# Performance work log

Measured on AMD Instinct MI355X. Metric: run time of the kernel, lower is better.

The kernel has to match this reference:

```python
import jax, jax.numpy as jnp
import numpy as np

N0, N1, N2 = 200000, 50000, 10000
E1, E2 = 800000, 160000
IN_F, HID, RANK, OUT_C = 128, 128, 64, 64


def _cp_graphconv(feat_src, feat_dst, src, dst, n_dst, W_src, W_dst, W_out, b):
    # CP-rank factorized GraphConv: project src feats to rank space, gather along
    # edges, mean-aggregate per dst node, multiply elementwise with dst rank
    # projection (CP / Hadamard fusion), then project to output space.
    h_src = feat_src @ W_src                      # [N_src, R]
    msg = h_src[src]                              # [E, R] gather
    agg = jax.ops.segment_sum(msg, dst, num_segments=n_dst)   # [n_dst, R]
    cnt = jax.ops.segment_sum(jnp.ones((dst.shape[0],), msg.dtype), dst, num_segments=n_dst)
    agg = agg / jnp.maximum(cnt, 1.0)[:, None]    # mean aggregation
    z = agg * (feat_dst @ W_dst)                  # [n_dst, R] CP hadamard
    return z @ W_out + b                          # [n_dst, out]


def setup_inputs() -> dict:
    key = jax.random.key(0)
    ks = jax.random.split(key, 12)
    s1 = 1.0 / np.sqrt(IN_F)
    s2 = 1.0 / np.sqrt(HID)
    sr = 1.0 / np.sqrt(RANK)
    return {
        "x": jax.random.normal(ks[0], (N0, IN_F), jnp.float32),
        "W_src1": jax.random.normal(ks[1], (IN_F, RANK), jnp.float32) * s1,
        "W_dst1": jax.random.normal(ks[2], (IN_F, RANK), jnp.float32) * s1,
        "W_out1": jax.random.normal(ks[3], (RANK, HID), jnp.float32) * sr,
        "b1": jnp.zeros((HID,), jnp.float32),
        "W_src2": jax.random.normal(ks[4], (HID, RANK), jnp.float32) * s2,
        "W_dst2": jax.random.normal(ks[5], (HID, RANK), jnp.float32) * s2,
        "W_out2": jax.random.normal(ks[6], (RANK, OUT_C), jnp.float32) * sr,
        "b2": jnp.zeros((OUT_C,), jnp.float32),
        "src1": jax.random.randint(ks[7], (E1,), 0, N0),
        "dst1": jax.random.randint(ks[8], (E1,), 0, N1),
        "src2": jax.random.randint(ks[9], (E2,), 0, N1),
        "dst2": jax.random.randint(ks[10], (E2,), 0, N2),
        "n_dst1": N1,
        "n_dst2": N2,
    }


def reference(x, W_src1, W_dst1, W_out1, b1, W_src2, W_dst2, W_out2, b2,
              src1, dst1, src2, dst2, n_dst1, n_dst2):
    h_dst = x[:n_dst1]
    h = _cp_graphconv(x, h_dst, src1, dst1, n_dst1, W_src1, W_dst1, W_out1, b1)
    h = jax.nn.relu(h)
    # dropout: eval mode (training=False) -> identity
    h_dst2 = h[:n_dst2]
    out = _cp_graphconv(h, h_dst2, src2, dst2, n_dst2, W_src2, W_dst2, W_out2, b2)
    return out
```

## Files before the change

### kernel.cpp

```cpp
#include <hip/hip_runtime.h>
#include <hip/hip_bf16.h>
#include <hip/hip_fp16.h>

#define N0 200000
#define N1 50000
#define N2 10000
#define E1C 800000
#define E2C 160000
#define NB1 784
#define NB2 160
#define NBT (NB1 + NB2)
#define CH1 64
#define CH2 16
#define NT1 3125
#define NT2 625

struct H4 { __half2 a, b; };
struct H8 { __half2 a, b, c, d; };

typedef _Float16 f16x8 __attribute__((ext_vector_type(8)));
typedef float f32x4 __attribute__((ext_vector_type(4)));
#define MFMA16(a, b, c) __builtin_amdgcn_mfma_f32_16x16x32_f16(a, b, c, 0, 0, 0)

#define WT_TOTAL 45056

__global__ __launch_bounds__(256) void prep(int4* __restrict__ histz,
                                            const float4* __restrict__ x4,
                                            H4* __restrict__ xh4,
                                            const float* __restrict__ Wsrc1,
                                            const float* __restrict__ Wdst1,
                                            const float* __restrict__ Wout1,
                                            const float* __restrict__ Wsrc2,
                                            const float* __restrict__ Wdst2,
                                            const float* __restrict__ Wout2,
                                            __half* __restrict__ wt) {
    const int NZ4 = NBT / 4;
    const int NC = N0 * 128 / 4;
    int i = blockIdx.x * 256 + threadIdx.x;
    if (i < NZ4) {
        histz[i] = make_int4(0, 0, 0, 0);
    } else {
        int j = i - NZ4;
        if (j < NC) {
            float4 v = x4[j];
            H4 o;
            o.a = __floats2half2_rn(v.x, v.y);
            o.b = __floats2half2_rn(v.z, v.w);
            xh4[j] = o;
        } else {
            int e = j - NC;
            if (e < WT_TOTAL) {
                float v;
                if (e < 8192)       { int e2 = e;         int n = e2 >> 7, k = e2 & 127; v = Wsrc1[k * 64 + n]; }
                else if (e < 16384) { int e2 = e - 8192;  int n = e2 >> 7, k = e2 & 127; v = Wdst1[k * 64 + n]; }
                else if (e < 24576) { int e2 = e - 16384; int n = e2 >> 6, k = e2 & 63;  v = Wout1[k * 128 + n]; }
                else if (e < 32768) { int e2 = e - 24576; int n = e2 >> 7, k = e2 & 127; v = Wsrc2[k * 64 + n]; }
                else if (e < 40960) { int e2 = e - 32768; int n = e2 >> 7, k = e2 & 127; v = Wdst2[k * 64 + n]; }
                else                { int e2 = e - 40960; int n = e2 >> 6, k = e2 & 63;  v = Wout2[k * 64 + n]; }
                wt[e] = __float2half(v);
            }
        }
    }
}

__global__ __launch_bounds__(256) void hist_k(const int* __restrict__ dst1,
                                              const int* __restrict__ dst2,
                                              int* __restrict__ hist) {
    __shared__ int hl[NB1];
    int b = blockIdx.x;
    const int* dst; int nb, goff, e0, e1;
    if (b < CH1) {
        dst = dst1; nb = NB1; goff = 0;
        int per = E1C / CH1 / 4;
        e0 = b * per; e1 = e0 + per;
    } else {
        dst = dst2; nb = NB2; goff = NB1;
        int per = E2C / CH2 / 4;
        int c = b - CH1;
        e0 = c * per; e1 = e0 + per;
    }
    for (int i = threadIdx.x; i < nb; i += 256) hl[i] = 0;
    __syncthreads();
    const int4* d4 = reinterpret_cast<const int4*>(dst);
    for (int i = e0 + threadIdx.x; i < e1; i += 256) {
        int4 v = d4[i];
        atomicAdd(&hl[v.x >> 6], 1);
        atomicAdd(&hl[v.y >> 6], 1);
        atomicAdd(&hl[v.z >> 6], 1);
        atomicAdd(&hl[v.w >> 6], 1);
    }
    __syncthreads();
    for (int i = threadIdx.x; i < nb; i += 256) {
        int c = hl[i];
        if (c) atomicAdd(&hist[goff + i], c);
    }
}

__global__ __launch_bounds__(1024) void scan_small(const int* __restrict__ hist,
                                                   int* __restrict__ base,
                                                   int* __restrict__ cursor) {
    int t = threadIdx.x, lane = t & 63, wid = t >> 6;
    int v = (t < NBT) ? hist[t] : 0;
    int s = v;
    #pragma unroll
    for (int o = 1; o < 64; o <<= 1) { int u = __shfl_up(s, o, 64); if (lane >= o) s += u; }
    __shared__ int ws[16];
    if (lane == 63) ws[wid] = s;
    __syncthreads();
    if (wid == 0 && lane < 16) {
        int w = ws[lane];
        #pragma unroll
        for (int o = 1; o < 16; o <<= 1) { int u = __shfl_up(w, o, 64); if (lane >= o) w += u; }
        ws[lane] = w;
    }
    __syncthreads();
    int excl = ((wid == 0) ? 0 : ws[wid - 1]) + (s - v);
    if (t < NBT) { base[t] = excl; cursor[t] = excl; }
}

__global__ __launch_bounds__(256) void scatter_k(const int* __restrict__ dst1,
                                                 const int* __restrict__ src1,
                                                 const int* __restrict__ dst2,
                                                 const int* __restrict__ src2,
                                                 int* __restrict__ cursor,
                                                 int* __restrict__ edgebuf) {
    __shared__ int cnt_l[98];
    __shared__ int rsv[98];
    __shared__ int cur_l[98];
    int b = blockIdx.x;
    const int* dst; const int* srcp; int goff, bpp, lo, e0, e1;
    if (b < 8 * CH1) {
        dst = dst1; srcp = src1; goff = 0; bpp = NB1 / 8;
        int part = b & 7, chunk = b >> 3;
        lo = part * bpp;
        int per = E1C / CH1 / 4;
        e0 = chunk * per; e1 = e0 + per;
    } else {
        int k = b - 8 * CH1;
        dst = dst2; srcp = src2; goff = NB1; bpp = NB2 / 8;
        int part = k & 7, chunk = k >> 3;
        lo = part * bpp;
        int per = E2C / CH2 / 4;
        e0 = chunk * per; e1 = e0 + per;
    }
    for (int i = threadIdx.x; i < bpp; i += 256) cnt_l[i] = 0;
    __syncthreads();
    const int4* d4 = reinterpret_cast<const int4*>(dst);
    const int4* s4 = reinterpret_cast<const int4*>(srcp);
    for (int i = e0 + threadIdx.x; i < e1; i += 256) {
        int4 v = d4[i];
        int b0 = (v.x >> 6) - lo; if ((unsigned)b0 < (unsigned)bpp) atomicAdd(&cnt_l[b0], 1);
        int b1 = (v.y >> 6) - lo; if ((unsigned)b1 < (unsigned)bpp) atomicAdd(&cnt_l[b1], 1);
        int b2 = (v.z >> 6) - lo; if ((unsigned)b2 < (unsigned)bpp) atomicAdd(&cnt_l[b2], 1);
        int b3 = (v.w >> 6) - lo; if ((unsigned)b3 < (unsigned)bpp) atomicAdd(&cnt_l[b3], 1);
    }
    __syncthreads();
    for (int i = threadIdx.x; i < bpp; i += 256) {
        int c = cnt_l[i];
        rsv[i] = c ? atomicAdd(&cursor[goff + lo + i], c) : 0;
        cur_l[i] = 0;
    }
    __syncthreads();
    for (int i = e0 + threadIdx.x; i < e1; i += 256) {
        int4 dv = d4[i];
        int4 sv = s4[i];
        int b0 = (dv.x >> 6) - lo;
        if ((unsigned)b0 < (unsigned)bpp) {
            int p = atomicAdd(&cur_l[b0], 1);
            edgebuf[rsv[b0] + p] = (sv.x << 6) | (dv.x & 63);
        }
        int b1 = (dv.y >> 6) - lo;
        if ((unsigned)b1 < (unsigned)bpp) {
            int p = atomicAdd(&cur_l[b1], 1);
            edgebuf[rsv[b1] + p] = (sv.y << 6) | (dv.y & 63);
        }
        int b2 = (dv.z >> 6) - lo;
        if ((unsigned)b2 < (unsigned)bpp) {
            int p = atomicAdd(&cur_l[b2], 1);
            edgebuf[rsv[b2] + p] = (sv.z << 6) | (dv.z & 63);
        }
        int b3 = (dv.w >> 6) - lo;
        if ((unsigned)b3 < (unsigned)bpp) {
            int p = atomicAdd(&cur_l[b3], 1);
            edgebuf[rsv[b3] + p] = (sv.w << 6) | (dv.w & 63);
        }
    }
}

__global__ __launch_bounds__(256) void seg_mean_b(const __half* __restrict__ X,
                                                  const int* __restrict__ edgebuf,
                                                  const int* __restrict__ base,
                                                  const int* __restrict__ hist,
                                                  __half* __restrict__ aggh,
                                                  int ndst, int gb0) {
    __shared__ int cnt_lds[64];
    __shared__ int ell[64 * 64];
    int bkt = blockIdx.x;
    int gb = gb0 + bkt;
    int ebase = base[gb];
    int ecnt = hist[gb];
    if (threadIdx.x < 64) cnt_lds[threadIdx.x] = 0;
    __syncthreads();
    for (int i = threadIdx.x; i < ecnt; i += 256) {
        int v = edgebuf[ebase + i];
        int ld = v & 63;
        int p = atomicAdd(&cnt_lds[ld], 1);
        if (p < 64) ell[(ld << 6) + p] = v >> 6;
    }
    __syncthreads();
    int wid = threadIdx.x >> 6, lane = threadIdx.x & 63;
    int sub = lane >> 4, fq = lane & 15;
    const H8* Xr = reinterpret_cast<const H8*>(X);
    for (int ld = wid; ld < 64; ld += 4) {
        int d = (bkt << 6) + ld;
        if (d >= ndst) continue;
        int cn = cnt_lds[ld];
        int m = cn < 64 ? cn : 64;
        float acc[8];
        #pragma unroll
        for (int i = 0; i < 8; ++i) acc[i] = 0.0f;
        for (int e = sub; e < m; e += 4) {
            int sidx = ell[(ld << 6) + e];
            H8 p = Xr[(size_t)sidx * 16 + fq];
            float2 f0 = __half22float2(p.a);
            float2 f1 = __half22float2(p.b);
            float2 f2 = __half22float2(p.c);
            float2 f3 = __half22float2(p.d);
            acc[0] += f0.x; acc[1] += f0.y; acc[2] += f1.x; acc[3] += f1.y;
            acc[4] += f2.x; acc[5] += f2.y; acc[6] += f3.x; acc[7] += f3.y;
        }
        #pragma unroll
        for (int o = 16; o <= 32; o <<= 1) {
            #pragma unroll
            for (int i = 0; i < 8; ++i) acc[i] += __shfl_xor(acc[i], o, 64);
        }
        if (sub == 0) {
            float inv = (cn > 0) ? (1.0f / (float)cn) : 0.0f;
            H8 o;
            o.a = __floats2half2_rn(acc[0] * inv, acc[1] * inv);
            o.b = __floats2half2_rn(acc[2] * inv, acc[3] * inv);
            o.c = __floats2half2_rn(acc[4] * inv, acc[5] * inv);
            o.d = __floats2half2_rn(acc[6] * inv, acc[7] * inv);
            *reinterpret_cast<H8*>(aggh + (size_t)d * 128 + fq * 8) = o;
        }
    }
}

__global__ __launch_bounds__(256) void layer1_mfma(const __half* __restrict__ aggh,
                                                   const __half* __restrict__ xh,
                                                   const __half* __restrict__ wth,
                                                   const float* __restrict__ b1,
                                                   __half* __restrict__ hh) {
    __shared__ _Float16 zt[4][16][72];
    int wave = threadIdx.x >> 6, lane = threadIdx.x & 63;
    int tile = blockIdx.x * 4 + wave;
    if (tile >= NT1) return;
    int r0 = tile * 16;
    int m = lane & 15, q = lane >> 4;
    const _Float16* A1 = (const _Float16*)aggh + (size_t)(r0 + m) * 128 + q * 8;
    const _Float16* A2 = (const _Float16*)xh   + (size_t)(r0 + m) * 128 + q * 8;
    const _Float16* wt = (const _Float16*)wth;
    const _Float16* Wsrc = wt;
    const _Float16* Wdst = wt + 8192;
    const _Float16* Wout = wt + 16384;

    f32x4 accA[4], accB[4];
    #pragma unroll
    for (int nt = 0; nt < 4; ++nt) { accA[nt] = (f32x4)(0.0f); accB[nt] = (f32x4)(0.0f); }
    #pragma unroll
    for (int kc = 0; kc < 4; ++kc) {
        f16x8 a1 = *(const f16x8*)(A1 + kc * 32);
        f16x8 a2 = *(const f16x8*)(A2 + kc * 32);
        #pragma unroll
        for (int nt = 0; nt < 4; ++nt) {
            f16x8 ba = *(const f16x8*)(Wsrc + (nt * 16 + m) * 128 + kc * 32 + q * 8);
            f16x8 bb = *(const f16x8*)(Wdst + (nt * 16 + m) * 128 + kc * 32 + q * 8);
            accA[nt] = MFMA16(a1, ba, accA[nt]);
            accB[nt] = MFMA16(a2, bb, accB[nt]);
        }
    }
    #pragma unroll
    for (int nt = 0; nt < 4; ++nt)
        #pragma unroll
        for (int i = 0; i < 4; ++i)
            zt[wave][q * 4 + i][nt * 16 + m] = (_Float16)(accA[nt][i] * accB[nt][i]);
    f32x4 acc2[8];
    #pragma unroll
    for (int nt = 0; nt < 8; ++nt) acc2[nt] = (f32x4)(0.0f);
    #pragma unroll
    for (int kc = 0; kc < 2; ++kc) {
        f16x8 az = *(const f16x8*)(&zt[wave][m][kc * 32 + q * 8]);
        #pragma unroll
        for (int nt = 0; nt < 8; ++nt) {
            f16x8 bo = *(const f16x8*)(Wout + (nt * 16 + m) * 64 + kc * 32 + q * 8);
            acc2[nt] = MFMA16(az, bo, acc2[nt]);
        }
    }
    #pragma unroll
    for (int nt = 0; nt < 8; ++nt) {
        float bz = b1[nt * 16 + m];
        #pragma unroll
        for (int i = 0; i < 4; ++i) {
            float v = fmaxf(acc2[nt][i] + bz, 0.0f);
            hh[(size_t)(r0 + q * 4 + i) * 128 + nt * 16 + m] = __float2half(v);
        }
    }
}

__global__ __launch_bounds__(256) void layer2_mfma(const __half* __restrict__ aggh,
                                                   const __half* __restrict__ hh,
                                                   const __half* __restrict__ wth,
                                                   const float* __restrict__ b2,
                                                   float* __restrict__ out) {
    __shared__ _Float16 zt[4][16][72];
    int wave = threadIdx.x >> 6, lane = threadIdx.x & 63;
    int tile = blockIdx.x * 4 + wave;
    if (tile >= NT2) return;
    int r0 = tile * 16;
    int m = lane & 15, q = lane >> 4;
    const _Float16* A1 = (const _Float16*)aggh + (size_t)(r0 + m) * 128 + q * 8;
    const _Float16* A2 = (const _Float16*)hh   + (size_t)(r0 + m) * 128 + q * 8;
    const _Float16* wt = (const _Float16*)wth;
    const _Float16* Wsrc = wt + 24576;
    const _Float16* Wdst = wt + 32768;
    const _Float16* Wout = wt + 40960;

    f32x4 accA[4], accB[4];
    #pragma unroll
    for (int nt = 0; nt < 4; ++nt) { accA[nt] = (f32x4)(0.0f); accB[nt] = (f32x4)(0.0f); }
    #pragma unroll
    for (int kc = 0; kc < 4; ++kc) {
        f16x8 a1 = *(const f16x8*)(A1 + kc * 32);
        f16x8 a2 = *(const f16x8*)(A2 + kc * 32);
        #pragma unroll
        for (int nt = 0; nt < 4; ++nt) {
            f16x8 ba = *(const f16x8*)(Wsrc + (nt * 16 + m) * 128 + kc * 32 + q * 8);
            f16x8 bb = *(const f16x8*)(Wdst + (nt * 16 + m) * 128 + kc * 32 + q * 8);
            accA[nt] = MFMA16(a1, ba, accA[nt]);
            accB[nt] = MFMA16(a2, bb, accB[nt]);
        }
    }
    #pragma unroll
    for (int nt = 0; nt < 4; ++nt)
        #pragma unroll
        for (int i = 0; i < 4; ++i)
            zt[wave][q * 4 + i][nt * 16 + m] = (_Float16)(accA[nt][i] * accB[nt][i]);
    f32x4 acc2[4];
    #pragma unroll
    for (int nt = 0; nt < 4; ++nt) acc2[nt] = (f32x4)(0.0f);
    #pragma unroll
    for (int kc = 0; kc < 2; ++kc) {
        f16x8 az = *(const f16x8*)(&zt[wave][m][kc * 32 + q * 8]);
        #pragma unroll
        for (int nt = 0; nt < 4; ++nt) {
            f16x8 bo = *(const f16x8*)(Wout + (nt * 16 + m) * 64 + kc * 32 + q * 8);
            acc2[nt] = MFMA16(az, bo, acc2[nt]);
        }
    }
    #pragma unroll
    for (int nt = 0; nt < 4; ++nt) {
        float bz = b2[nt * 16 + m];
        #pragma unroll
        for (int i = 0; i < 4; ++i)
            out[(size_t)(r0 + q * 4 + i) * 64 + nt * 16 + m] = acc2[nt][i] + bz;
    }
}

extern "C" void kernel_launch(void* const* d_in, const int* in_sizes, int n_in,
                              void* d_out, int out_size, void* d_ws, size_t ws_size,
                              hipStream_t stream) {
    const float* x     = (const float*)d_in[0];
    const float* Wsrc1 = (const float*)d_in[1];
    const float* Wdst1 = (const float*)d_in[2];
    const float* Wout1 = (const float*)d_in[3];
    const float* b1    = (const float*)d_in[4];
    const float* Wsrc2 = (const float*)d_in[5];
    const float* Wdst2 = (const float*)d_in[6];
    const float* Wout2 = (const float*)d_in[7];
    const float* b2    = (const float*)d_in[8];
    const int* src1    = (const int*)d_in[9];
    const int* dst1    = (const int*)d_in[10];
    const int* src2    = (const int*)d_in[11];
    const int* dst2    = (const int*)d_in[12];
    float* out = (float*)d_out;

    char* basep = (char*)d_ws;
    __half* xh    = (__half*)(basep);
    __half* agg1h = (__half*)(basep + 51200000);
    __half* hh    = (__half*)(basep + 64000000);
    __half* agg2h = (__half*)(basep + 76800000);
    int* hist    = (int*)(basep + 79360000);
    int* bbase   = hist + NBT;
    int* cursor  = bbase + NBT;
    int* edgebuf = cursor + NBT;
    __half* wt   = (__half*)(basep + 83211328);

    {
        int total = NBT / 4 + N0 * 128 / 4 + WT_TOTAL;
        prep<<<(total + 255) / 256, 256, 0, stream>>>((int4*)hist, (const float4*)x, (H4*)xh,
                                                      Wsrc1, Wdst1, Wout1, Wsrc2, Wdst2, Wout2, wt);
    }
    hist_k<<<CH1 + CH2, 256, 0, stream>>>(dst1, dst2, hist);
    scan_small<<<1, 1024, 0, stream>>>(hist, bbase, cursor);
    scatter_k<<<8 * CH1 + 8 * CH2, 256, 0, stream>>>(dst1, src1, dst2, src2, cursor, edgebuf);

    seg_mean_b<<<NB1, 256, 0, stream>>>(xh, edgebuf, bbase, hist, agg1h, N1, 0);
    layer1_mfma<<<(NT1 + 3) / 4, 256, 0, stream>>>(agg1h, xh, wt, b1, hh);

    seg_mean_b<<<157, 256, 0, stream>>>(hh, edgebuf, bbase, hist, agg2h, N2, NB1);
    layer2_mfma<<<(NT2 + 3) / 4, 256, 0, stream>>>(agg2h, hh, wt, b2, out);
}
```

Measured before the change: 327.3 us.

## Project source features to rank space before gathering instead of after aggregation

Reorders each layer so features are multiplied by W_src (128->64) before the edge gather and mean. The gather and segment mean now move 64-wide half rows instead of 128-wide, and the full fp32->fp16 copy of x is replaced by a fused projection kernel that reads x directly. Layer 1 also computes the layer-2 source and destination projections in its epilogue. In exchange, the W_src projection now runs on all 200k source rows rather than only the 50k destination rows, and rounding to half happens at a different point.

Result: faster. 310.9 us (-5.0%).

```diff
diff --git a/kernel.cpp b/kernel.cpp
--- a/kernel.cpp
+++ b/kernel.cpp
@@ -12,10 +12,10 @@
 #define NBT (NB1 + NB2)
 #define CH1 64
 #define CH2 16
+#define NTP 12500
 #define NT1 3125
 #define NT2 625
 
-struct H4 { __half2 a, b; };
 struct H8 { __half2 a, b, c, d; };
 
 typedef _Float16 f16x8 __attribute__((ext_vector_type(8)));
@@ -24,41 +24,29 @@
 
 #define WT_TOTAL 45056
 
-__global__ __launch_bounds__(256) void prep(int4* __restrict__ histz,
-                                            const float4* __restrict__ x4,
-                                            H4* __restrict__ xh4,
-                                            const float* __restrict__ Wsrc1,
-                                            const float* __restrict__ Wdst1,
-                                            const float* __restrict__ Wout1,
-                                            const float* __restrict__ Wsrc2,
-                                            const float* __restrict__ Wdst2,
-                                            const float* __restrict__ Wout2,
-                                            __half* __restrict__ wt) {
+__global__ __launch_bounds__(256) void prep_small(int4* __restrict__ histz,
+                                                  const float* __restrict__ Wsrc1,
+                                                  const float* __restrict__ Wdst1,
+                                                  const float* __restrict__ Wout1,
+                                                  const float* __restrict__ Wsrc2,
+                                                  const float* __restrict__ Wdst2,
+                                                  const float* __restrict__ Wout2,
+                                                  __half* __restrict__ wt) {
     const int NZ4 = NBT / 4;
-    const int NC = N0 * 128 / 4;
     int i = blockIdx.x * 256 + threadIdx.x;
     if (i < NZ4) {
         histz[i] = make_int4(0, 0, 0, 0);
     } else {
-        int j = i - NZ4;
-        if (j < NC) {
-            float4 v = x4[j];
-            H4 o;
-            o.a = __floats2half2_rn(v.x, v.y);
-            o.b = __floats2half2_rn(v.z, v.w);
-            xh4[j] = o;
-        } else {
-            int e = j - NC;
-            if (e < WT_TOTAL) {
-                float v;
-                if (e < 8192)       { int e2 = e;         int n = e2 >> 7, k = e2 & 127; v = Wsrc1[k * 64 + n]; }
-                else if (e < 16384) { int e2 = e - 8192;  int n = e2 >> 7, k = e2 & 127; v = Wdst1[k * 64 + n]; }
-                else if (e < 24576) { int e2 = e - 16384; int n = e2 >> 6, k = e2 & 63;  v = Wout1[k * 128 + n]; }
-                else if (e < 32768) { int e2 = e - 24576; int n = e2 >> 7, k = e2 & 127; v = Wsrc2[k * 64 + n]; }
-                else if (e < 40960) { int e2 = e - 32768; int n = e2 >> 7, k = e2 & 127; v = Wdst2[k * 64 + n]; }
-                else                { int e2 = e - 40960; int n = e2 >> 6, k = e2 & 63;  v = Wout2[k * 64 + n]; }
-                wt[e] = __float2half(v);
-            }
+        int e = i - NZ4;
+        if (e < WT_TOTAL) {
+            float v;
+            if (e < 8192)       { int e2 = e;         int n = e2 >> 7, k = e2 & 127; v = Wsrc1[k * 64 + n]; }
+            else if (e < 16384) { int e2 = e - 8192;  int n = e2 >> 7, k = e2 & 127; v = Wdst1[k * 64 + n]; }
+            else if (e < 24576) { int e2 = e - 16384; int n = e2 >> 6, k = e2 & 63;  v = Wout1[k * 128 + n]; }
+            else if (e < 32768) { int e2 = e - 24576; int n = e2 >> 7, k = e2 & 127; v = Wsrc2[k * 64 + n]; }
+            else if (e < 40960) { int e2 = e - 32768; int n = e2 >> 7, k = e2 & 127; v = Wdst2[k * 64 + n]; }
+            else                { int e2 = e - 40960; int n = e2 >> 6, k = e2 & 63;  v = Wout2[k * 64 + n]; }
+            wt[e] = __float2half(v);
         }
     }
 }
@@ -187,7 +175,66 @@
     }
 }
 
-__global__ __launch_bounds__(256) void seg_mean_b(const __half* __restrict__ X,
+__global__ __launch_bounds__(256) void proj1(const float* __restrict__ x,
+                                             const __half* __restrict__ wth,
+                                             __half* __restrict__ hsrc,
+                                             __half* __restrict__ hdst) {
+    int wave = threadIdx.x >> 6, lane = threadIdx.x & 63;
+    int tile = blockIdx.x * 4 + wave;
+    if (tile >= NTP) return;
+    int r0 = tile * 16;
+    int m = lane & 15, q = lane >> 4;
+    const float* A = x + (size_t)(r0 + m) * 128 + q * 8;
+    const _Float16* wt = (const _Float16*)wth;
+    const _Float16* Wsrc = wt;
+    const _Float16* Wdst = wt + 8192;
+
+    f16x8 a[4];
+    #pragma unroll
+    for (int kc = 0; kc < 4; ++kc) {
+        float4 v0 = *(const float4*)(A + kc * 32);
+        float4 v1 = *(const float4*)(A + kc * 32 + 4);
+        f16x8 t;
+        t[0] = (_Float16)v0.x; t[1] = (_Float16)v0.y; t[2] = (_Float16)v0.z; t[3] = (_Float16)v0.w;
+        t[4] = (_Float16)v1.x; t[5] = (_Float16)v1.y; t[6] = (_Float16)v1.z; t[7] = (_Float16)v1.w;
+        a[kc] = t;
+    }
+    f32x4 accS[4];
+    #pragma unroll
+    for (int nt = 0; nt < 4; ++nt) accS[nt] = (f32x4)(0.0f);
+    #pragma unroll
+    for (int kc = 0; kc < 4; ++kc)
+        #pragma unroll
+        for (int nt = 0; nt < 4; ++nt) {
+            f16x8 b = *(const f16x8*)(Wsrc + (nt * 16 + m) * 128 + kc * 32 + q * 8);
+            accS[nt] = MFMA16(a[kc], b, accS[nt]);
+        }
+    #pragma unroll
+    for (int nt = 0; nt < 4; ++nt)
+        #pragma unroll
+        for (int i = 0; i < 4; ++i)
+            hsrc[(size_t)(r0 + q * 4 + i) * 64 + nt * 16 + m] = __float2half(accS[nt][i]);
+
+    if (tile < NT1) {
+        f32x4 accD[4];
+        #pragma unroll
+        for (int nt = 0; nt < 4; ++nt) accD[nt] = (f32x4)(0.0f);
+        #pragma unroll
+        for (int kc = 0; kc < 4; ++kc)
+            #pragma unroll
+            for (int nt = 0; nt < 4; ++nt) {
+                f16x8 b = *(const f16x8*)(Wdst + (nt * 16 + m) * 128 + kc * 32 + q * 8);
+                accD[nt] = MFMA16(a[kc], b, accD[nt]);
+            }
+        #pragma unroll
+        for (int nt = 0; nt < 4; ++nt)
+            #pragma unroll
+            for (int i = 0; i < 4; ++i)
+                hdst[(size_t)(r0 + q * 4 + i) * 64 + nt * 16 + m] = __float2half(accD[nt][i]);
+    }
+}
+
+__global__ __launch_bounds__(256) void seg_mean64(const __half* __restrict__ X,
                                                   const int* __restrict__ edgebuf,
                                                   const int* __restrict__ base,
                                                   const int* __restrict__ hist,
@@ -209,19 +256,19 @@
     }
     __syncthreads();
     int wid = threadIdx.x >> 6, lane = threadIdx.x & 63;
-    int sub = lane >> 4, fq = lane & 15;
+    int sub = lane >> 3, fq = lane & 7;
     const H8* Xr = reinterpret_cast<const H8*>(X);
     for (int ld = wid; ld < 64; ld += 4) {
         int d = (bkt << 6) + ld;
         if (d >= ndst) continue;
         int cn = cnt_lds[ld];
-        int m = cn < 64 ? cn : 64;
+        int mm = cn < 64 ? cn : 64;
         float acc[8];
         #pragma unroll
         for (int i = 0; i < 8; ++i) acc[i] = 0.0f;
-        for (int e = sub; e < m; e += 4) {
+        for (int e = sub; e < mm; e += 8) {
             int sidx = ell[(ld << 6) + e];
-            H8 p = Xr[(size_t)sidx * 16 + fq];
+            H8 p = Xr[(size_t)sidx * 8 + fq];
             float2 f0 = __half22float2(p.a);
             float2 f1 = __half22float2(p.b);
             float2 f2 = __half22float2(p.c);
@@ -230,7 +277,7 @@
             acc[4] += f2.x; acc[5] += f2.y; acc[6] += f3.x; acc[7] += f3.y;
         }
         #pragma unroll
-        for (int o = 16; o <= 32; o <<= 1) {
+        for (int o = 8; o <= 32; o <<= 1) {
             #pragma unroll
             for (int i = 0; i < 8; ++i) acc[i] += __shfl_xor(acc[i], o, 64);
         }
@@ -241,59 +288,44 @@
             o.b = __floats2half2_rn(acc[2] * inv, acc[3] * inv);
             o.c = __floats2half2_rn(acc[4] * inv, acc[5] * inv);
             o.d = __floats2half2_rn(acc[6] * inv, acc[7] * inv);
-            *reinterpret_cast<H8*>(aggh + (size_t)d * 128 + fq * 8) = o;
-        }
-    }
-}
-
-__global__ __launch_bounds__(256) void layer1_mfma(const __half* __restrict__ aggh,
-                                                   const __half* __restrict__ xh,
-                                                   const __half* __restrict__ wth,
-                                                   const float* __restrict__ b1,
-                                                   __half* __restrict__ hh) {
-    __shared__ _Float16 zt[4][16][72];
+            *reinterpret_cast<H8*>(aggh + (size_t)d * 64 + fq * 8) = o;
+        }
+    }
+}
+
+__global__ __launch_bounds__(256) void layer1_k(const __half* __restrict__ agg1,
+                                                const __half* __restrict__ hdst1,
+                                                const __half* __restrict__ wth,
+                                                const float* __restrict__ b1,
+                                                __half* __restrict__ hsrc2,
+                                                __half* __restrict__ hdst2) {
+    __shared__ _Float16 zt[4][16][136];
     int wave = threadIdx.x >> 6, lane = threadIdx.x & 63;
     int tile = blockIdx.x * 4 + wave;
     if (tile >= NT1) return;
     int r0 = tile * 16;
     int m = lane & 15, q = lane >> 4;
-    const _Float16* A1 = (const _Float16*)aggh + (size_t)(r0 + m) * 128 + q * 8;
-    const _Float16* A2 = (const _Float16*)xh   + (size_t)(r0 + m) * 128 + q * 8;
+    const _Float16* Az = (const _Float16*)agg1  + (size_t)(r0 + m) * 64 + q * 8;
+    const _Float16* Ad = (const _Float16*)hdst1 + (size_t)(r0 + m) * 64 + q * 8;
     const _Float16* wt = (const _Float16*)wth;
-    const _Float16* Wsrc = wt;
-    const _Float16* Wdst = wt + 8192;
-    const _Float16* Wout = wt + 16384;
-
-    f32x4 accA[4], accB[4];
-    #pragma unroll
-    for (int nt = 0; nt < 4; ++nt) { accA[nt] = (f32x4)(0.0f); accB[nt] = (f32x4)(0.0f); }
-    #pragma unroll
-    for (int kc = 0; kc < 4; ++kc) {
-        f16x8 a1 = *(const f16x8*)(A1 + kc * 32);
-        f16x8 a2 = *(const f16x8*)(A2 + kc * 32);
-        #pragma unroll
-        for (int nt = 0; nt < 4; ++nt) {
-            f16x8 ba = *(const f16x8*)(Wsrc + (nt * 16 + m) * 128 + kc * 32 + q * 8);
-            f16x8 bb = *(const f16x8*)(Wdst + (nt * 16 + m) * 128 + kc * 32 + q * 8);
-            accA[nt] = MFMA16(a1, ba, accA[nt]);
-            accB[nt] = MFMA16(a2, bb, accB[nt]);
-        }
-    }
-    #pragma unroll
-    for (int nt = 0; nt < 4; ++nt)
-        #pragma unroll
-        for (int i = 0; i < 4; ++i)
-            zt[wave][q * 4 + i][nt * 16 + m] = (_Float16)(accA[nt][i] * accB[nt][i]);
+    const _Float16* Wout  = wt + 16384;
+    const _Float16* Wsrc2 = wt + 24576;
+    const _Float16* Wdst2 = wt + 32768;
+
     f32x4 acc2[8];
     #pragma unroll
     for (int nt = 0; nt < 8; ++nt) acc2[nt] = (f32x4)(0.0f);
     #pragma unroll
     for (int kc = 0; kc < 2; ++kc) {
-        f16x8 az = *(const f16x8*)(&zt[wave][m][kc * 32 + q * 8]);
+        f16x8 az = *(const f16x8*)(Az + kc * 32);
+        f16x8 ad = *(const f16x8*)(Ad + kc * 32);
+        f16x8 z;
+        #pragma unroll
+        for (int i = 0; i < 8; ++i) z[i] = (_Float16)((float)az[i] * (float)ad[i]);
         #pragma unroll
         for (int nt = 0; nt < 8; ++nt) {
             f16x8 bo = *(const f16x8*)(Wout + (nt * 16 + m) * 64 + kc * 32 + q * 8);
-            acc2[nt] = MFMA16(az, bo, acc2[nt]);
+            acc2[nt] = MFMA16(z, bo, acc2[nt]);
         }
     }
     #pragma unroll
@@ -302,59 +334,71 @@
         #pragma unroll
         for (int i = 0; i < 4; ++i) {
             float v = fmaxf(acc2[nt][i] + bz, 0.0f);
-            hh[(size_t)(r0 + q * 4 + i) * 128 + nt * 16 + m] = __float2half(v);
-        }
-    }
-}
-
-__global__ __launch_bounds__(256) void layer2_mfma(const __half* __restrict__ aggh,
-                                                   const __half* __restrict__ hh,
-                                                   const __half* __restrict__ wth,
-                                                   const float* __restrict__ b2,
-                                                   float* __restrict__ out) {
-    __shared__ _Float16 zt[4][16][72];
+            zt[wave][q * 4 + i][nt * 16 + m] = (_Float16)v;
+        }
+    }
+    f32x4 accS[4], accD[4];
+    #pragma unroll
+    for (int nt = 0; nt < 4; ++nt) { accS[nt] = (f32x4)(0.0f); accD[nt] = (f32x4)(0.0f); }
+    bool do_dst = (tile < NT2);
+    #pragma unroll
+    for (int kc = 0; kc < 4; ++kc) {
+        f16x8 ah = *(const f16x8*)(&zt[wave][m][kc * 32 + q * 8]);
+        #pragma unroll
+        for (int nt = 0; nt < 4; ++nt) {
+            f16x8 bs = *(const f16x8*)(Wsrc2 + (nt * 16 + m) * 128 + kc * 32 + q * 8);
+            accS[nt] = MFMA16(ah, bs, accS[nt]);
+        }
+        if (do_dst) {
+            #pragma unroll
+            for (int nt = 0; nt < 4; ++nt) {
+                f16x8 bd = *(const f16x8*)(Wdst2 + (nt * 16 + m) * 128 + kc * 32 + q * 8);
+                accD[nt] = MFMA16(ah, bd, accD[nt]);
+            }
+        }
+    }
+    #pragma unroll
+    for (int nt = 0; nt < 4; ++nt)
+        #pragma unroll
+        for (int i = 0; i < 4; ++i)
+            hsrc2[(size_t)(r0 + q * 4 + i) * 64 + nt * 16 + m] = __float2half(accS[nt][i]);
+    if (do_dst) {
+        #pragma unroll
+        for (int nt = 0; nt < 4; ++nt)
+            #pragma unroll
+            for (int i = 0; i < 4; ++i)
+                hdst2[(size_t)(r0 + q * 4 + i) * 64 + nt * 16 + m] = __float2half(accD[nt][i]);
+    }
+}
+
+__global__ __launch_bounds__(256) void layer2_k(const __half* __restrict__ agg2,
+                                                const __half* __restrict__ hdst2,
+                                                const __half* __restrict__ wth,
+                                                const float* __restrict__ b2,
+                                                float* __restrict__ out) {
     int wave = threadIdx.x >> 6, lane = threadIdx.x & 63;
     int tile = blockIdx.x * 4 + wave;
     if (tile >= NT2) return;
     int r0 = tile * 16;
     int m = lane & 15, q = lane >> 4;
-    const _Float16* A1 = (const _Float16*)aggh + (size_t)(r0 + m) * 128 + q * 8;
-    const _Float16* A2 = (const _Float16*)hh   + (size_t)(r0 + m) * 128 + q * 8;
-    const _Float16* wt = (const _Float16*)wth;
-    const _Float16* Wsrc = wt + 24576;
-    const _Float16* Wdst = wt + 32768;
-    const _Float16* Wout = wt + 40960;
-
-    f32x4 accA[4], accB[4];
-    #pragma unroll
-    for (int nt = 0; nt < 4; ++nt) { accA[nt] = (f32x4)(0.0f); accB[nt] = (f32x4)(0.0f); }
-    #pragma unroll
-    for (int kc = 0; kc < 4; ++kc) {
-        f16x8 a1 = *(const f16x8*)(A1 + kc * 32);
-        f16x8 a2 = *(const f16x8*)(A2 + kc * 32);
-        #pragma unroll
-        for (int nt = 0; nt < 4; ++nt) {
-            f16x8 ba = *(const f16x8*)(Wsrc + (nt * 16 + m) * 128 + kc * 32 + q * 8);
-            f16x8 bb = *(const f16x8*)(Wdst + (nt * 16 + m) * 128 + kc * 32 + q * 8);
-            accA[nt] = MFMA16(a1, ba, accA[nt]);
-            accB[nt] = MFMA16(a2, bb, accB[nt]);
-        }
-    }
-    #pragma unroll
-    for (int nt = 0; nt < 4; ++nt)
-        #pragma unroll
-        for (int i = 0; i < 4; ++i)
-            zt[wave][q * 4 + i][nt * 16 + m] = (_Float16)(accA[nt][i] * accB[nt][i]);
-    f32x4 acc2[4];
-    #pragma unroll
-    for (int nt = 0; nt < 4; ++nt) acc2[nt] = (f32x4)(0.0f);
+    const _Float16* Az = (const _Float16*)agg2  + (size_t)(r0 + m) * 64 + q * 8;
+    const _Float16* Ad = (const _Float16*)hdst2 + (size_t)(r0 + m) * 64 + q * 8;
+    const _Float16* Wout = (const _Float16*)wth + 40960;
+
+    f32x4 acc[4];
+    #pragma unroll
+    for (int nt = 0; nt < 4; ++nt) acc[nt] = (f32x4)(0.0f);
     #pragma unroll
     for (int kc = 0; kc < 2; ++kc) {
-        f16x8 az = *(const f16x8*)(&zt[wave][m][kc * 32 + q * 8]);
+        f16x8 az = *(const f16x8*)(Az + kc * 32);
+        f16x8 ad = *(const f16x8*)(Ad + kc * 32);
+        f16x8 z;
+        #pragma unroll
+        for (int i = 0; i < 8; ++i) z[i] = (_Float16)((float)az[i] * (float)ad[i]);
         #pragma unroll
         for (int nt = 0; nt < 4; ++nt) {
             f16x8 bo = *(const f16x8*)(Wout + (nt * 16 + m) * 64 + kc * 32 + q * 8);
-            acc2[nt] = MFMA16(az, bo, acc2[nt]);
+            acc[nt] = MFMA16(z, bo, acc[nt]);
         }
     }
     #pragma unroll
@@ -362,7 +406,7 @@
         float bz = b2[nt * 16 + m];
         #pragma unroll
         for (int i = 0; i < 4; ++i)
-            out[(size_t)(r0 + q * 4 + i) * 64 + nt * 16 + m] = acc2[nt][i] + bz;
+            out[(size_t)(r0 + q * 4 + i) * 64 + nt * 16 + m] = acc[nt][i] + bz;
     }
 }
 
@@ -385,28 +429,31 @@
     float* out = (float*)d_out;
 
     char* basep = (char*)d_ws;
-    __half* xh    = (__half*)(basep);
-    __half* agg1h = (__half*)(basep + 51200000);
-    __half* hh    = (__half*)(basep + 64000000);
-    __half* agg2h = (__half*)(basep + 76800000);
-    int* hist    = (int*)(basep + 79360000);
+    __half* hsrc1 = (__half*)(basep);
+    __half* hdst1 = (__half*)(basep + 25600000);
+    __half* agg1  = (__half*)(basep + 32000000);
+    __half* hsrc2 = (__half*)(basep + 38400000);
+    __half* hdst2 = (__half*)(basep + 44800000);
+    __half* agg2  = (__half*)(basep + 46080000);
+    int* hist    = (int*)(basep + 47360000);
     int* bbase   = hist + NBT;
     int* cursor  = bbase + NBT;
-    int* edgebuf = cursor + NBT;
-    __half* wt   = (__half*)(basep + 83211328);
+    int* edgebuf = (int*)(basep + 47371328);
+    __half* wt   = (__half*)(basep + 51211328);
 
     {
-        int total = NBT / 4 + N0 * 128 / 4 + WT_TOTAL;
-        prep<<<(total + 255) / 256, 256, 0, stream>>>((int4*)hist, (const float4*)x, (H4*)xh,
-                                                      Wsrc1, Wdst1, Wout1, Wsrc2, Wdst2, Wout2, wt);
+        int total = NBT / 4 + WT_TOTAL;
+        prep_small<<<(total + 255) / 256, 256, 0, stream>>>((int4*)hist,
+                                                            Wsrc1, Wdst1, Wout1, Wsrc2, Wdst2, Wout2, wt);
     }
     hist_k<<<CH1 + CH2, 256, 0, stream>>>(dst1, dst2, hist);
     scan_small<<<1, 1024, 0, stream>>>(hist, bbase, cursor);
     scatter_k<<<8 * CH1 + 8 * CH2, 256, 0, stream>>>(dst1, src1, dst2, src2, cursor, edgebuf);
 
-    seg_mean_b<<<NB1, 256, 0, stream>>>(xh, edgebuf, bbase, hist, agg1h, N1, 0);
-    layer1_mfma<<<(NT1 + 3) / 4, 256, 0, stream>>>(agg1h, xh, wt, b1, hh);
-
-    seg_mean_b<<<157, 256, 0, stream>>>(hh, edgebuf, bbase, hist, agg2h, N2, NB1);
-    layer2_mfma<<<(NT2 + 3) / 4, 256, 0, stream>>>(agg2h, hh, wt, b2, out);
-}
+    proj1<<<(NTP + 3) / 4, 256, 0, stream>>>(x, wt, hsrc1, hdst1);
+    seg_mean64<<<782, 256, 0, stream>>>(hsrc1, edgebuf, bbase, hist, agg1, N1, 0);
+    layer1_k<<<(NT1 + 3) / 4, 256, 0, stream>>>(agg1, hdst1, wt, b1, hsrc2, hdst2);
+
+    seg_mean64<<<157, 256, 0, stream>>>(hsrc2, edgebuf, bbase, hist, agg2, N2, NB1);
+    layer2_k<<<(NT2 + 3) / 4, 256, 0, stream>>>(agg2, hdst2, wt, b2, out);
+}
```
